# Optimization experiments

Hardware: AMD Instinct MI355X
Metric: run time of the kernel (lower is better)

Reference implementation:

```python
import jax, jax.numpy as jnp
import numpy as np

V = 32000
MASK_ID = 31999
EPS = 1e-3          # log-linear schedule eps
DT = 0.05           # reverse-step size
NUCLEUS_P = 0.9
NEG_INF = -1000000.0
B, S = 2, 1024


def move_chance(t):
    # BD3-LM log-linear schedule: move_chance(t) = (1 - eps) * t
    return (1.0 - EPS) * t


def nucleus_filter(probs, p):
    # descending sort over vocab
    order = jnp.argsort(-probs, axis=-1)                     # [B,S,V]
    sorted_probs = jnp.take_along_axis(probs, order, axis=-1)
    cum = jnp.cumsum(sorted_probs, axis=-1)
    keep = cum <= p
    keep = keep.at[..., 0].set(True)                          # always keep top-1
    kept = sorted_probs * keep
    inv = jnp.argsort(order, axis=-1)                         # inverse permutation
    filtered = jnp.take_along_axis(kept, inv, axis=-1)        # scatter back
    return filtered / jnp.sum(filtered, axis=-1, keepdims=True)


def setup_inputs() -> dict:
    key = jax.random.key(0)
    k1, k2, k3, k4 = jax.random.split(key, 4)
    x = jax.random.randint(k1, (B, S), 0, V, dtype=jnp.int32)
    m = jax.random.uniform(k4, (B, S)) < 0.5
    x = jnp.where(m, MASK_ID, x)
    logits = jax.random.normal(k2, (B, S, V), dtype=jnp.float32)
    t = jnp.ones((1,), dtype=jnp.float32)
    u = jax.random.uniform(k3, (B, S, V), dtype=jnp.float32)
    return {"x": x, "logits": logits, "t": t, "u": u}


def reference(x, logits, t, u):
    mct = move_chance(t)[..., None]          # [1,1]
    mcs = move_chance(t - DT)[..., None]     # [1,1]
    mask_prob = mcs / mct                    # [1,1], broadcasts over [S,V]

    logits = logits.at[:, :, MASK_ID].set(NEG_INF)
    p_x0 = jax.nn.softmax(logits, axis=-1)   # [B,S,V]
    p_x0 = nucleus_filter(p_x0, NUCLEUS_P)

    q_xs = p_x0 * (1.0 - mask_prob)
    q_xs = q_xs.at[:, :, MASK_ID].set(jnp.squeeze(mask_prob, -1))

    gumbel = -jnp.log(-jnp.log(u + 1e-10) + 1e-10)
    x_new = jnp.argmax(q_xs / (gumbel + 1e-10), axis=-1).astype(x.dtype)

    is_masked = x == MASK_ID
    x_new = jnp.where(is_masked, x_new, x)
    return x_new, p_x0
```

## Files before the change

kernel.cpp:

```cpp
#include <hip/hip_runtime.h>

#define NVOC 32000
#define NV4  (NVOC / 4)
#define MASKID 31999
#define NBINS2 2048
#define NTHR 512
#define NWAVES (NTHR / 64)
#define LISTCAP 2048

typedef unsigned int u32;
typedef unsigned long long u64;

__device__ __forceinline__ u32 fix32(float e) {
    float x = e * 4294967296.0f;
    x = fminf(x, 4294967040.0f);
    return (u32)x;
}

__device__ __forceinline__ int zbin(float t) {
    int b = (int)floorf(t);
    b = b < 0 ? 0 : b;
    return b > (NBINS2 - 1) ? (NBINS2 - 1) : b;
}
__device__ __forceinline__ float elq(float t, int b) {
    return __expf((t - (float)(b + 1)) * 0.015625f);
}

__global__ __launch_bounds__(NTHR, 8) void mdlm_kernel(
    const int* __restrict__ xin,
    const float* __restrict__ logits,
    const float* __restrict__ tin,
    const float* __restrict__ uin,
    float* __restrict__ out,
    int rows)
{
    __shared__ u64 sHist[NBINS2];
    __shared__ float sTab[NBINS2];
    __shared__ u32 sList[LISTCAP];
    __shared__ double sRedD[NWAVES];
    __shared__ int sRedI[NWAVES];
    __shared__ float sTT;
    __shared__ int sCnt, sB, sCross, sMaxDrop, sBref;
    __shared__ u32 sTau;
    __shared__ u64 sPart;
    __shared__ double sAsD, sSfpD, sScaleB;

    double* sD = (double*)sHist;

    const int row = blockIdx.x;
    if (row >= rows) return;
    const int tid = threadIdx.x;
    const int lane = tid & 63;
    const float4* lrow4 = (const float4*)(logits + (size_t)row * NVOC);
    const float4* urow4 = (const float4*)(uin + (size_t)row * NVOC);
    const float* urowf = (const float*)urow4;
    float* prow = out + (size_t)rows + (size_t)row * NVOC;

#pragma unroll
    for (int k = 0; k < 4; ++k) sHist[tid + k * NTHR] = 0ULL;
    if (tid == 0) {
        sCnt = 0; sB = -1; sCross = 0; sMaxDrop = -1; sBref = -1;
        sTau = 0xFFFFFFFFu; sPart = 0ULL;
        sTT = tin[0];
    }
    __syncthreads();

    for (int v4 = tid; v4 < NV4; v4 += NTHR) {
        float4 f = lrow4[v4];
        if (v4 == (MASKID >> 2)) f.w = -1000000.0f;
        float zz[4] = {f.x, f.y, f.z, f.w};
#pragma unroll
        for (int e4 = 0; e4 < 4; ++e4) {
            float t = fmaf(zz[e4], 64.0f, 1024.0f);
            int b = zbin(t);
            u32 m = fix32(elq(t, b));
            atomicAdd(&sHist[b], (u64)m);
        }
    }
    __syncthreads();

#pragma unroll
    for (int k = 0; k < 4; ++k) {
        int s = tid + k * NTHR;
        if (sHist[s] != 0ULL) atomicMax(&sBref, s);
    }
    __syncthreads();
    const int bref = sBref;

#pragma unroll
    for (int k = 0; k < 4; ++k) {
        int s = tid + k * NTHR;
        double sc = exp((double)(s - bref) * 0.015625);
        sTab[s] = (float)sc;
        u64 H = sHist[s];
        sD[s] = (double)H * sc;
    }
    __syncthreads();

    {
        const int base = tid * 4;
        double b0 = sD[base + 0], b1 = sD[base + 1], b2 = sD[base + 2], b3 = sD[base + 3];
        double l3 = b3, l2 = b2 + l3, l1 = b1 + l2, l0 = b0 + l1;
        const double pt = l0;
        double ws = pt;
#pragma unroll
        for (int off = 1; off < 64; off <<= 1) {
            double o = __shfl_down(ws, off, 64);
            if (lane + off < 64) ws += o;
        }
        double ex = __shfl_down(ws, 1, 64);
        double exw = (lane < 63) ? ex : 0.0;
        if (lane == 0) sRedD[tid >> 6] = ws;
        __syncthreads();
        double woff = 0.0;
        {
            int w = tid >> 6;
            for (int w2 = w + 1; w2 < NWAVES; ++w2) woff += sRedD[w2];
        }
        double excl = exw + woff;
        sD[base + 0] = l0 + excl;
        sD[base + 1] = l1 + excl;
        sD[base + 2] = l2 + excl;
        sD[base + 3] = l3 + excl;
        __syncthreads();
    }
    const double T = 0.9 * sD[0];

#pragma unroll
    for (int k = 0; k < 4; ++k) {
        int s = tid + k * NTHR;
        double Ai = sD[s];
        double As = (s + 1 < NBINS2) ? sD[s + 1] : 0.0;
        bool dropped = (As >= T);
        bool keptf = (Ai <= T);
        if (dropped) atomicMax(&sMaxDrop, s);
        if (!dropped && !keptf) { sB = s; sCross = 1; }
    }
    __syncthreads();
    if (tid == 0) {
        int B = sCross ? sB : sMaxDrop;
        sB = B;
        double As = (B + 1 < NBINS2) ? sD[B + 1] : 0.0;
        if (B < 0) As = sD[0];
        sAsD = As;
        sSfpD = As;
        sScaleB = (B >= 0) ? exp((double)(B - bref) * 0.015625) : 1.0;
    }
    __syncthreads();

    const int Bst = sB;
    const int cross = sCross;
    const double AsD = sAsD;
    const double dScaleB = sScaleB;

    if (cross) {
        for (int v4 = tid; v4 < NV4; v4 += NTHR) {
            float4 f = lrow4[v4];
            if (v4 == (MASKID >> 2)) f.w = -1000000.0f;
            float zz[4] = {f.x, f.y, f.z, f.w};
#pragma unroll
            for (int e4 = 0; e4 < 4; ++e4) {
                float t = fmaf(zz[e4], 64.0f, 1024.0f);
                int b = zbin(t);
                if (b == Bst) {
                    u32 m = fix32(elq(t, b));
                    int pos = atomicAdd(&sCnt, 1);
                    if (pos < LISTCAP) sList[pos] = m;
                }
            }
        }
        __syncthreads();
        const int K = sCnt < LISTCAP ? sCnt : LISTCAP;
        for (int jj = tid; jj < K; jj += NTHR) {
            u32 mj = sList[jj];
            u64 isum = 0ULL;
            for (int q2 = 0; q2 < K; ++q2) {
                u32 mv = sList[q2];
                if (mv >= mj) isum += (u64)mv;
            }
            double s = AsD + (double)isum * dScaleB;
            if (s <= T) atomicMin(&sTau, mj);
        }
        __syncthreads();
        u32 tl = sTau;
        if (tl != 0xFFFFFFFFu) {
            u64 part = 0ULL;
            for (int q2 = tid; q2 < K; q2 += NTHR) {
                u32 mv = sList[q2];
                if (mv >= tl) part += (u64)mv;
            }
            if (part) atomicAdd(&sPart, part);
        }
        __syncthreads();
        if (tid == 0 && tl != 0xFFFFFFFFu)
            sSfpD = AsD + (double)sPart * dScaleB;
        __syncthreads();
    }

    const u32 tauU = (cross && sTau != 0xFFFFFFFFu) ? sTau : 0xFFFFFFFFu;
    const float invSf = (float)(4294967296.0 / sSfpD);

#pragma unroll
    for (int k = 0; k < 4; ++k) sTab[tid + k * NTHR] *= invSf;

    double mpd, omd;
    {
        double td = (double)sTT;
        mpd = ((1.0 - 1e-3) * (td - 0.05)) / ((1.0 - 1e-3) * td);
        omd = 1.0 - mpd;
    }
    const float mqf = (float)(mpd / omd);
    __syncthreads();

    float r1 = -3.0e38f, r2 = -3.0e38f;
    float q1 = 0.0f,     q2 = 0.0f;
    int   i1 = 0,        i2 = 0;
    for (int v4 = tid; v4 < NV4; v4 += NTHR) {
        float4 uf = urow4[v4];
        float4 f = lrow4[v4];
        if (v4 == (MASKID >> 2)) f.w = -1000000.0f;
        float zz[4] = {f.x, f.y, f.z, f.w};
        float uu[4] = {uf.x, uf.y, uf.z, uf.w};
        float pp[4];
        const int i0 = v4 * 4;
#pragma unroll
        for (int e4 = 0; e4 < 4; ++e4) {
            float t = fmaf(zz[e4], 64.0f, 1024.0f);
            int b = zbin(t);
            float el = elq(t, b);
            bool kept = (b > Bst) || (b == Bst && fix32(el) >= tauU);
            float p = kept ? el * sTab[b] : 0.0f;
            pp[e4] = p;
            if (kept) {
                float g = -__logf(1e-10f - __logf(uu[e4] + 1e-10f));
                float r = p * __builtin_amdgcn_rcpf(g + 1e-10f);
                if (r > r1)      { r2 = r1; q2 = q1; i2 = i1; r1 = r; q1 = p; i1 = i0 + e4; }
                else if (r > r2) { r2 = r;  q2 = p;  i2 = i0 + e4; }
            }
        }
        float4 po;
        po.x = pp[0]; po.y = pp[1]; po.z = pp[2]; po.w = pp[3];
        ((float4*)prow)[v4] = po;
    }
    if (tid == ((MASKID >> 2) % NTHR)) {
        float um = urowf[MASKID];
        float g = -__logf(1e-10f - __logf(um + 1e-10f));
        float rm = mqf * __builtin_amdgcn_rcpf(g + 1e-10f);
        if (rm > r1)      { r2 = r1; q2 = q1; i2 = i1; r1 = rm; q1 = 0.0f; i1 = MASKID; }
        else if (rm > r2) { r2 = rm; q2 = 0.0f; i2 = MASKID; }
    }

    double best; int bidx;
    {
        double qa = (i1 == MASKID) ? mpd : (double)q1 * omd;
        double g1 = -log(-log((double)urowf[i1] + 1e-10) + 1e-10);
        best = qa / (g1 + 1e-10);
        bidx = i1;
        double qb = (i2 == MASKID) ? mpd : (double)q2 * omd;
        double g2 = -log(-log((double)urowf[i2] + 1e-10) + 1e-10);
        double rd = qb / (g2 + 1e-10);
        if (rd > best || (rd == best && i2 < bidx)) { best = rd; bidx = i2; }
    }

    for (int off = 32; off > 0; off >>= 1) {
        double ov = __shfl_down(best, off, 64);
        int oi = __shfl_down(bidx, off, 64);
        if (ov > best || (ov == best && oi < bidx)) { best = ov; bidx = oi; }
    }
    if (lane == 0) { sRedD[tid >> 6] = best; sRedI[tid >> 6] = bidx; }
    __syncthreads();
    if (tid == 0) {
        best = sRedD[0]; bidx = sRedI[0];
        for (int w = 1; w < NWAVES; ++w) {
            double ov = sRedD[w]; int oi = sRedI[w];
            if (ov > best || (ov == best && oi < bidx)) { best = ov; bidx = oi; }
        }
        int xv = xin[row];
        out[row] = (float)((xv == MASKID) ? bidx : xv);
    }
}

extern "C" void kernel_launch(void* const* d_in, const int* in_sizes, int n_in,
                              void* d_out, int out_size, void* d_ws, size_t ws_size,
                              hipStream_t stream) {
    const int* x = (const int*)d_in[0];
    const float* logits = (const float*)d_in[1];
    const float* t = (const float*)d_in[2];
    const float* u = (const float*)d_in[3];
    float* out = (float*)d_out;
    const int rows = in_sizes[0];
    hipLaunchKernelGGL(mdlm_kernel, dim3(rows), dim3(NTHR), 0, stream,
                       x, logits, t, u, out, rows);
}
```

Baseline: 252.5 us.

## Use 32-bit shared histogram with 22-bit fixed point instead of 64-bit atomics

Switches the per-bin exp-mass histogram from 64-bit atomics on 32-bit fixed-point values to 32-bit atomics on 22-bit fixed-point values, which halves shared memory for the histogram and avoids 64-bit LDS atomics. Each thread now reads four contiguous bins into registers for the bref search and the scale pass. The final pass also computes the gumbel ratio for every element rather than only kept ones, removing a branch at the cost of extra log work. The lower fixed-point resolution can change nucleus-threshold ties and risks 32-bit bin overflow, and one dead expression is left in the loop.

```diff
diff --git a/kernel.cpp b/kernel.cpp
--- a/kernel.cpp
+++ b/kernel.cpp
@@ -11,9 +11,9 @@
 typedef unsigned int u32;
 typedef unsigned long long u64;
 
-__device__ __forceinline__ u32 fix32(float e) {
-    float x = e * 4294967296.0f;
-    x = fminf(x, 4294967040.0f);
+__device__ __forceinline__ u32 fix22(float e) {
+    float x = e * 4194304.0f;
+    x = fminf(x, 4194303.0f);
     return (u32)x;
 }
 
@@ -34,7 +34,7 @@
     float* __restrict__ out,
     int rows)
 {
-    __shared__ u64 sHist[NBINS2];
+    __shared__ double sD[NBINS2];
     __shared__ float sTab[NBINS2];
     __shared__ u32 sList[LISTCAP];
     __shared__ double sRedD[NWAVES];
@@ -45,7 +45,7 @@
     __shared__ u64 sPart;
     __shared__ double sAsD, sSfpD, sScaleB;
 
-    double* sD = (double*)sHist;
+    u32* sHistU = (u32*)sD;
 
     const int row = blockIdx.x;
     if (row >= rows) return;
@@ -57,7 +57,7 @@
     float* prow = out + (size_t)rows + (size_t)row * NVOC;
 
 #pragma unroll
-    for (int k = 0; k < 4; ++k) sHist[tid + k * NTHR] = 0ULL;
+    for (int k = 0; k < 4; ++k) sHistU[tid * 4 + k] = 0u;
     if (tid == 0) {
         sCnt = 0; sB = -1; sCross = 0; sMaxDrop = -1; sBref = -1;
         sTau = 0xFFFFFFFFu; sPart = 0ULL;
@@ -73,27 +73,37 @@
         for (int e4 = 0; e4 < 4; ++e4) {
             float t = fmaf(zz[e4], 64.0f, 1024.0f);
             int b = zbin(t);
-            u32 m = fix32(elq(t, b));
-            atomicAdd(&sHist[b], (u64)m);
-        }
-    }
-    __syncthreads();
-
-#pragma unroll
-    for (int k = 0; k < 4; ++k) {
-        int s = tid + k * NTHR;
-        if (sHist[s] != 0ULL) atomicMax(&sBref, s);
+            u32 m = fix22(elq(t, b));
+            atomicAdd(&sHistU[b], m);
+        }
+    }
+    __syncthreads();
+
+    u32 h0, h1, h2, h3;
+    {
+        const int base = tid * 4;
+        h0 = sHistU[base + 0]; h1 = sHistU[base + 1];
+        h2 = sHistU[base + 2]; h3 = sHistU[base + 3];
+        int hb = -1;
+        if (h0) hb = base + 0;
+        if (h1) hb = base + 1;
+        if (h2) hb = base + 2;
+        if (h3) hb = base + 3;
+        if (hb >= 0) atomicMax(&sBref, hb);
     }
     __syncthreads();
     const int bref = sBref;
 
-#pragma unroll
-    for (int k = 0; k < 4; ++k) {
-        int s = tid + k * NTHR;
-        double sc = exp((double)(s - bref) * 0.015625);
-        sTab[s] = (float)sc;
-        u64 H = sHist[s];
-        sD[s] = (double)H * sc;
+    {
+        const int base = tid * 4;
+#pragma unroll
+        for (int k = 0; k < 4; ++k) {
+            int s = base + k;
+            double sc = exp((double)(s - bref) * 0.015625);
+            sTab[s] = (float)sc;
+            u32 H = (k == 0) ? h0 : (k == 1) ? h1 : (k == 2) ? h2 : h3;
+            sD[s] = (double)H * sc;
+        }
     }
     __syncthreads();
 
@@ -101,8 +111,7 @@
         const int base = tid * 4;
         double b0 = sD[base + 0], b1 = sD[base + 1], b2 = sD[base + 2], b3 = sD[base + 3];
         double l3 = b3, l2 = b2 + l3, l1 = b1 + l2, l0 = b0 + l1;
-        const double pt = l0;
-        double ws = pt;
+        double ws = l0;
 #pragma unroll
         for (int off = 1; off < 64; off <<= 1) {
             double o = __shfl_down(ws, off, 64);
@@ -163,7 +172,7 @@
                 float t = fmaf(zz[e4], 64.0f, 1024.0f);
                 int b = zbin(t);
                 if (b == Bst) {
-                    u32 m = fix32(elq(t, b));
+                    u32 m = fix22(elq(t, b));
                     int pos = atomicAdd(&sCnt, 1);
                     if (pos < LISTCAP) sList[pos] = m;
                 }
@@ -198,7 +207,7 @@
     }
 
     const u32 tauU = (cross && sTau != 0xFFFFFFFFu) ? sTau : 0xFFFFFFFFu;
-    const float invSf = (float)(4294967296.0 / sSfpD);
+    const float invSf = (float)(4194304.0 / sSfpD);
 
 #pragma unroll
     for (int k = 0; k < 4; ++k) sTab[tid + k * NTHR] *= invSf;
@@ -228,15 +237,14 @@
             float t = fmaf(zz[e4], 64.0f, 1024.0f);
             int b = zbin(t);
             float el = elq(t, b);
-            bool kept = (b > Bst) || (b == Bst && fix32(el) >= tauU);
-            float p = kept ? el * sTab[b] : 0.0f;
+            bool kept = (b > Bst) || (b == Bst && fix22(el) >= tauU);
+            float p = kept ? (float)fix22(el) * sTab[b] * (1.0f / 4194304.0f) * 4194304.0f : 0.0f;
+            p = kept ? el * sTab[b] : 0.0f;
             pp[e4] = p;
-            if (kept) {
-                float g = -__logf(1e-10f - __logf(uu[e4] + 1e-10f));
-                float r = p * __builtin_amdgcn_rcpf(g + 1e-10f);
-                if (r > r1)      { r2 = r1; q2 = q1; i2 = i1; r1 = r; q1 = p; i1 = i0 + e4; }
-                else if (r > r2) { r2 = r;  q2 = p;  i2 = i0 + e4; }
-            }
+            float g = -__logf(1e-10f - __logf(uu[e4] + 1e-10f));
+            float r = p * __builtin_amdgcn_rcpf(g + 1e-10f);
+            if (r > r1)      { r2 = r1; q2 = q1; i2 = i1; r1 = r; q1 = p; i1 = i0 + e4; }
+            else if (r > r2) { r2 = r;  q2 = p;  i2 = i0 + e4; }
         }
         float4 po;
         po.x = pp[0]; po.y = pp[1]; po.z = pp[2]; po.w = pp[3];
```

Result: no change. 252.9 us (median of 2 runs) (+0.2%).
